# Optimization experiments

Measured on AMD Instinct MI355X. Metric: run time of the kernel, lower is better.

Reference implementation:

```python
import jax, jax.numpy as jnp
import numpy as np

N = 8192


def setup_inputs() -> dict:
    key = jax.random.key(0)
    k1, k2, k3, k4, k5, k6 = jax.random.split(key, 6)
    return {
        "t": jnp.zeros((1,), dtype=jnp.float32),
        "state": jax.random.uniform(k1, (3 * N,), dtype=jnp.float32),
        "betas": jax.random.uniform(k2, (N,), dtype=jnp.float32),
        "deltas": jax.random.uniform(k3, (N,), dtype=jnp.float32),
        "cs": jax.random.uniform(k4, (N,), dtype=jnp.float32),
        "ps": jax.random.uniform(k5, (N,), dtype=jnp.float32),
        "ts": jax.random.uniform(k6, (N, N), dtype=jnp.float32),
    }


def reference(t, state, betas, deltas, cs, ps, ts):
    # state is interleaved (U_0, I_0, V_0, U_1, I_1, V_1, ...)
    s = state.reshape(N, 3)
    U, I, V = s[:, 0], s[:, 1], s[:, 2]
    # squared_parametrization applied to per-host rate parameters
    beta = jnp.square(betas)
    delta = jnp.square(deltas)
    c = jnp.square(cs)
    p = jnp.square(ps)

    infect = beta * U * V  # (N,)
    dU = -infect
    dI = infect - delta * I
    # neighbor sum over nbr != n of ts[nbr, n] * V[nbr]  ==  ts^T @ V - diag(ts) * V
    coupling = ts.T @ V - jnp.diagonal(ts) * V
    dV = p * I - c * V + coupling

    return jnp.stack([dU, dI, dV], axis=1).reshape(-1)
```

## Files before the change

### kernel.cpp

```cpp
#include <hip/hip_runtime.h>

#define NN 8192
#define S1_BLOCKS 512
#define ROWS_PER_BLOCK (NN / S1_BLOCKS)

__global__ __launch_bounds__(256) void partial_matvec(
    const float* __restrict__ ts,
    const float* __restrict__ state,
    float* __restrict__ ws)
{
    const int b = blockIdx.x;
    const int t = threadIdx.x;
    const int r0 = b * ROWS_PER_BLOCK;

    float4 acc[8];
#pragma unroll
    for (int s = 0; s < 8; ++s) acc[s] = make_float4(0.f, 0.f, 0.f, 0.f);

    const float* base = ts + (size_t)r0 * NN + t * 4;
    for (int r = 0; r < ROWS_PER_BLOCK; ++r) {
        float v = state[3 * (r0 + r) + 2];
        const float* rowp = base + (size_t)r * NN;
#pragma unroll
        for (int s = 0; s < 8; ++s) {
            float4 x = *(const float4*)(rowp + s * 1024);
            acc[s].x += x.x * v;
            acc[s].y += x.y * v;
            acc[s].z += x.z * v;
            acc[s].w += x.w * v;
        }
    }

    float* wsb = ws + (size_t)b * NN + t * 4;
#pragma unroll
    for (int s = 0; s < 8; ++s)
        *(float4*)(wsb + s * 1024) = acc[s];
}

__global__ __launch_bounds__(256) void finalize_kernel(
    const float* __restrict__ ws,
    const float* __restrict__ state,
    const float* __restrict__ betas,
    const float* __restrict__ deltas,
    const float* __restrict__ cs,
    const float* __restrict__ ps,
    const float* __restrict__ ts,
    float* __restrict__ out)
{
    const int bb = blockIdx.x;
    const int t  = threadIdx.x;
    const int cl = t & 31;
    const int g  = t >> 5;
    const int col = bb * 32 + cl;

    float sum = 0.f;
    const float* p = ws + (size_t)(g * 64) * NN + col;
#pragma unroll 8
    for (int k = 0; k < 64; ++k)
        sum += p[(size_t)k * NN];

    __shared__ float red[8][32];
    red[g][cl] = sum;
    __syncthreads();

    if (t < 32) {
        float coupling = 0.f;
#pragma unroll
        for (int g2 = 0; g2 < 8; ++g2) coupling += red[g2][t];

        const int j = bb * 32 + t;
        float U = state[3 * j + 0];
        float I = state[3 * j + 1];
        float V = state[3 * j + 2];
        float beta  = betas[j]  * betas[j];
        float delta = deltas[j] * deltas[j];
        float c     = cs[j]     * cs[j];
        float pp    = ps[j]     * ps[j];
        float diag  = ts[(size_t)j * NN + j];
        float infect = beta * U * V;
        out[3 * j + 0] = -infect;
        out[3 * j + 1] = infect - delta * I;
        out[3 * j + 2] = pp * I - c * V - diag * V + coupling;
    }
}

extern "C" void kernel_launch(void* const* d_in, const int* in_sizes, int n_in,
                              void* d_out, int out_size, void* d_ws, size_t ws_size,
                              hipStream_t stream) {
    const float* state  = (const float*)d_in[1];
    const float* betas  = (const float*)d_in[2];
    const float* deltas = (const float*)d_in[3];
    const float* cs     = (const float*)d_in[4];
    const float* ps     = (const float*)d_in[5];
    const float* ts     = (const float*)d_in[6];
    float* out = (float*)d_out;
    float* ws  = (float*)d_ws;

    partial_matvec<<<S1_BLOCKS, 256, 0, stream>>>(ts, state, ws);
    finalize_kernel<<<NN / 32, 256, 0, stream>>>(ws, state, betas, deltas,
                                                 cs, ps, ts, out);
}
```

Before: 374.8 us.

## Double-buffer row loads in matvec, widen blocks, vectorize finalize reduction

The partial matvec kernel now uses 512 threads, each owning 4 float4 column chunks instead of 8. It preloads all 16 V values and software-pipelines the next row's loads while accumulating the current row, to hide memory latency. The finalize kernel reads the workspace as float4 so each block handles 128 columns, which cuts the number of blocks and scalar loads. The cost is more registers per thread and a larger block size, which may lower occupancy.

After: 373.2 us. No clear change (-0.4%).

```diff
diff --git a/kernel.cpp b/kernel.cpp
--- a/kernel.cpp
+++ b/kernel.cpp
@@ -2,39 +2,59 @@
 
 #define NN 8192
 #define S1_BLOCKS 512
-#define ROWS_PER_BLOCK (NN / S1_BLOCKS)
+#define ROWS 16
 
-__global__ __launch_bounds__(256) void partial_matvec(
+__global__ __launch_bounds__(512) void partial_matvec(
     const float* __restrict__ ts,
     const float* __restrict__ state,
     float* __restrict__ ws)
 {
     const int b = blockIdx.x;
     const int t = threadIdx.x;
-    const int r0 = b * ROWS_PER_BLOCK;
+    const int r0 = b * ROWS;
 
-    float4 acc[8];
+    float v[ROWS];
 #pragma unroll
-    for (int s = 0; s < 8; ++s) acc[s] = make_float4(0.f, 0.f, 0.f, 0.f);
+    for (int r = 0; r < ROWS; ++r)
+        v[r] = state[3 * (r0 + r) + 2];
 
     const float* base = ts + (size_t)r0 * NN + t * 4;
-    for (int r = 0; r < ROWS_PER_BLOCK; ++r) {
-        float v = state[3 * (r0 + r) + 2];
-        const float* rowp = base + (size_t)r * NN;
+
+    float4 acc[4], cur[4];
 #pragma unroll
-        for (int s = 0; s < 8; ++s) {
-            float4 x = *(const float4*)(rowp + s * 1024);
-            acc[s].x += x.x * v;
-            acc[s].y += x.y * v;
-            acc[s].z += x.z * v;
-            acc[s].w += x.w * v;
+    for (int s = 0; s < 4; ++s) {
+        acc[s] = make_float4(0.f, 0.f, 0.f, 0.f);
+        cur[s] = *(const float4*)(base + s * 2048);
+    }
+
+    for (int r = 0; r < ROWS - 1; ++r) {
+        float4 nxt[4];
+        const float* nrow = base + (size_t)(r + 1) * NN;
+#pragma unroll
+        for (int s = 0; s < 4; ++s)
+            nxt[s] = *(const float4*)(nrow + s * 2048);
+#pragma unroll
+        for (int s = 0; s < 4; ++s) {
+            acc[s].x += cur[s].x * v[r];
+            acc[s].y += cur[s].y * v[r];
+            acc[s].z += cur[s].z * v[r];
+            acc[s].w += cur[s].w * v[r];
         }
+#pragma unroll
+        for (int s = 0; s < 4; ++s) cur[s] = nxt[s];
+    }
+#pragma unroll
+    for (int s = 0; s < 4; ++s) {
+        acc[s].x += cur[s].x * v[ROWS - 1];
+        acc[s].y += cur[s].y * v[ROWS - 1];
+        acc[s].z += cur[s].z * v[ROWS - 1];
+        acc[s].w += cur[s].w * v[ROWS - 1];
     }
 
     float* wsb = ws + (size_t)b * NN + t * 4;
 #pragma unroll
-    for (int s = 0; s < 8; ++s)
-        *(float4*)(wsb + s * 1024) = acc[s];
+    for (int s = 0; s < 4; ++s)
+        *(float4*)(wsb + s * 2048) = acc[s];
 }
 
 __global__ __launch_bounds__(256) void finalize_kernel(
@@ -49,26 +69,30 @@
 {
     const int bb = blockIdx.x;
     const int t  = threadIdx.x;
-    const int cl = t & 31;
+    const int f4 = t & 31;
     const int g  = t >> 5;
-    const int col = bb * 32 + cl;
 
-    float sum = 0.f;
-    const float* p = ws + (size_t)(g * 64) * NN + col;
+    const float4* ws4 = (const float4*)ws;
+    const float4* p = ws4 + (size_t)(g * 64) * 2048 + bb * 32 + f4;
+
+    float4 sum = make_float4(0.f, 0.f, 0.f, 0.f);
 #pragma unroll 8
-    for (int k = 0; k < 64; ++k)
-        sum += p[(size_t)k * NN];
+    for (int k = 0; k < 64; ++k) {
+        float4 x = p[(size_t)k * 2048];
+        sum.x += x.x; sum.y += x.y; sum.z += x.z; sum.w += x.w;
+    }
 
-    __shared__ float red[8][32];
-    red[g][cl] = sum;
+    __shared__ float4 red[8][32];
+    red[g][f4] = sum;
     __syncthreads();
 
-    if (t < 32) {
+    if (t < 128) {
+        const int j = bb * 128 + t;
         float coupling = 0.f;
 #pragma unroll
-        for (int g2 = 0; g2 < 8; ++g2) coupling += red[g2][t];
+        for (int g2 = 0; g2 < 8; ++g2)
+            coupling += ((const float*)&red[g2][t >> 2])[t & 3];
 
-        const int j = bb * 32 + t;
         float U = state[3 * j + 0];
         float I = state[3 * j + 1];
         float V = state[3 * j + 2];
@@ -96,7 +120,7 @@
     float* out = (float*)d_out;
     float* ws  = (float*)d_ws;
 
-    partial_matvec<<<S1_BLOCKS, 256, 0, stream>>>(ts, state, ws);
-    finalize_kernel<<<NN / 32, 256, 0, stream>>>(ws, state, betas, deltas,
-                                                 cs, ps, ts, out);
+    partial_matvec<<<S1_BLOCKS, 512, 0, stream>>>(ts, state, ws);
+    finalize_kernel<<<NN / 128, 256, 0, stream>>>(ws, state, betas, deltas,
+                                                  cs, ps, ts, out);
 }
```
